# Optimization experiments

Hardware: AMD Instinct MI355X
Metric: run time of the kernel (lower is better)

## Reference

```python
import jax, jax.numpy as jnp
import numpy as np


def _lstm_cell(gates, c_prev):
    # PyTorch gate order: input, forget, cell(g), output
    i, f, g, o = jnp.split(gates, 4, axis=-1)
    c = jax.nn.sigmoid(f) * c_prev + jax.nn.sigmoid(i) * jnp.tanh(g)
    h = jax.nn.sigmoid(o) * jnp.tanh(c)
    return h, c


def setup_inputs() -> dict:
    key = jax.random.key(0)
    ks = jax.random.split(key, 20)
    s = 0.1
    x = jax.random.normal(ks[0], (1, 1, 37), dtype=jnp.float32)
    # active flags live at columns 12 + 5*opp_id; set opponents 0,2,3 active (==1)
    act_idx = 12 + 5 * jnp.arange(5)
    flags = jnp.array([1.0, 0.0, 1.0, 1.0, 0.0], dtype=jnp.float32)
    x = x.at[0, 0, act_idx].set(flags)
    inp = {
        'x': x,
        'gen_Wih': s * jax.random.normal(ks[1], (10, 40, 12), dtype=jnp.float32),
        'gen_Whh': s * jax.random.normal(ks[2], (10, 40, 10), dtype=jnp.float32),
        'gen_bih': s * jax.random.normal(ks[3], (10, 40), dtype=jnp.float32),
        'gen_bhh': s * jax.random.normal(ks[4], (10, 40), dtype=jnp.float32),
        'gen_h0': s * jax.random.normal(ks[5], (10, 10), dtype=jnp.float32),
        'gen_c0': s * jax.random.normal(ks[6], (10, 10), dtype=jnp.float32),
        'game_Wih': s * jax.random.normal(ks[7], (5, 10, 20, 4), dtype=jnp.float32),
        'game_Whh': s * jax.random.normal(ks[8], (5, 10, 20, 5), dtype=jnp.float32),
        'game_bih': s * jax.random.normal(ks[9], (5, 10, 20), dtype=jnp.float32),
        'game_bhh': s * jax.random.normal(ks[10], (5, 10, 20), dtype=jnp.float32),
        'game_h0': s * jax.random.normal(ks[11], (5, 10, 5), dtype=jnp.float32),
        'game_c0': s * jax.random.normal(ks[12], (5, 10, 5), dtype=jnp.float32),
        'W1': s * jax.random.normal(ks[13], (50, 200), dtype=jnp.float32),
        'b1': s * jax.random.normal(ks[14], (50,), dtype=jnp.float32),
        'W2': s * jax.random.normal(ks[15], (10, 50), dtype=jnp.float32),
        'b2': s * jax.random.normal(ks[16], (10,), dtype=jnp.float32),
        'W3': s * jax.random.normal(ks[17], (1, 10), dtype=jnp.float32),
        'b3': s * jax.random.normal(ks[18], (1,), dtype=jnp.float32),
    }
    return inp


def reference(x, gen_Wih, gen_Whh, gen_bih, gen_bhh, gen_h0, gen_c0,
              game_Wih, game_Whh, game_bih, game_bhh, game_h0, game_c0,
              W1, b1, W2, b2, W3, b3):
    # seq_len = batch = 1 (forced by the view(1,1,-1) -> Linear(200) shapes)
    xg = x[0, 0, :12]                                     # [12] general features
    # 10 independent LSTM(12,10) cells, batched via einsum over the cell axis k
    gates_g = (jnp.einsum('kgd,d->kg', gen_Wih, xg)
               + jnp.einsum('kgh,kh->kg', gen_Whh, gen_h0)
               + gen_bih + gen_bhh)                       # [10, 40]
    h_gen, _ = _lstm_cell(gates_g, gen_c0)                # [10, 10]
    x_gen_out = h_gen.reshape(-1)                         # [100]

    xo = x[0, 0, 12:37].reshape(5, 5)                     # 5 opponents x 5 feats
    active = xo[:, 0]                                     # active flag
    feats = xo[:, 1:]                                     # [5, 4]
    # 5 opponents x 10 independent LSTM(4,5) game cells
    gates_o = (jnp.einsum('okgd,od->okg', game_Wih, feats)
               + jnp.einsum('okgh,okh->okg', game_Whh, game_h0)
               + game_bih + game_bhh)                     # [5, 10, 20]
    h_game, _ = _lstm_cell(gates_o, game_c0)              # [5, 10, 5]
    game_flat = h_game.reshape(5, 50)
    # Bug replicated from source: the round loop concatenates x_opp_game (the
    # stale output of game-LSTM #9) 10 times; round LSTM outputs are unused.
    repeated = jnp.tile(h_game[:, 9, :], (1, 10))         # [5, 50]
    opp_single = jnp.concatenate([game_flat, repeated], axis=1)  # [5, 100]

    mask = (active == 1.0).astype(x.dtype)                # 'if x_active == 1'
    opp_avg = (mask[:, None] * opp_single).sum(0) / mask.sum()   # mean over active

    test = jnp.concatenate([x_gen_out, opp_avg])          # [200]
    h1 = jnp.tanh(test @ W1.T + b1)
    h2 = jnp.tanh(h1 @ W2.T + b2)
    out = jnp.tanh(h2 @ W3.T + b3)
    return out.reshape(1, 1, 1)
```

## Files before the change

kernel.cpp:

```cpp
#include <hip/hip_runtime.h>
#include <math.h>


__device__ __forceinline__ float fsig(float v) {
    return __fdividef(1.0f, 1.0f + __expf(-v));
}
__device__ __forceinline__ float ftanh(float v) {
    return 1.0f - __fdividef(2.0f, 1.0f + __expf(2.0f * v));
}

__global__ __launch_bounds__(384) void net6max_kernel(
    const float* __restrict__ x,
    const float* __restrict__ gen_Wih,
    const float* __restrict__ gen_Whh,
    const float* __restrict__ gen_bih,
    const float* __restrict__ gen_bhh,
    const float* __restrict__ gen_h0,
    const float* __restrict__ gen_c0,
    const float* __restrict__ game_Wih,
    const float* __restrict__ game_Whh,
    const float* __restrict__ game_bih,
    const float* __restrict__ game_bhh,
    const float* __restrict__ game_h0,
    const float* __restrict__ game_c0,
    const float* __restrict__ W1,
    const float* __restrict__ b1,
    const float* __restrict__ W2,
    const float* __restrict__ b2,
    const float* __restrict__ W3,
    const float* __restrict__ b3,
    float* __restrict__ out)
{
    __shared__ __align__(16) float s_hgame[5][10][5];
    __shared__ __align__(16) float s_test[200];
    __shared__ __align__(16) float s_h1[52];

    const int tid = threadIdx.x;

    if (tid < 100) {
        int k = tid / 10, j = tid % 10;
        const float*  Wk  = gen_Wih + (size_t)k * 480;
        const float*  Uk  = gen_Whh + (size_t)k * 400;
        const float*  bi  = gen_bih + k * 40;
        const float*  bh  = gen_bhh + k * 40;
        const float2* h02 = (const float2*)(gen_h0 + k * 10);
        float2 h0a = h02[0], h0b = h02[1], h0c = h02[2], h0d = h02[3], h0e = h02[4];
        float4 xa = *(const float4*)&x[0];
        float4 xb = *(const float4*)&x[4];
        float4 xc = *(const float4*)&x[8];
        float g4[4];
        #pragma unroll
        for (int gq = 0; gq < 4; ++gq) {
            int r = gq * 10 + j;
            const float4* w4 = (const float4*)(Wk + r * 12);
            const float2* u2 = (const float2*)(Uk + r * 10);
            float4 p = w4[0] * xa + w4[1] * xb + w4[2] * xc;
            float2 q = u2[0] * h0a + u2[1] * h0b + u2[2] * h0c
                     + u2[3] * h0d + u2[4] * h0e;
            g4[gq] = bi[r] + bh[r] + p.x + p.y + p.z + p.w + q.x + q.y;
        }
        float c = fsig(g4[1]) * gen_c0[tid] + fsig(g4[0]) * ftanh(g4[2]);
        s_test[tid] = fsig(g4[3]) * ftanh(c);
    } else if (tid >= 128 && tid < 378) {
        int u = tid - 128;
        int o = u / 50;
        int rem = u % 50;
        int k = rem / 5, j = rem % 5;
        int ok = o * 10 + k;
        const float* Wk = game_Wih + (size_t)ok * 80;
        const float* Uk = game_Whh + (size_t)ok * 100;
        const float* bi = game_bih + ok * 20;
        const float* bh = game_bhh + ok * 20;
        const float* h0 = game_h0 + ok * 5;
        float h00 = h0[0], h01 = h0[1], h02_ = h0[2], h03 = h0[3], h04 = h0[4];
        const float* fx = x + 13 + 5 * o;
        float f0 = fx[0], f1 = fx[1], f2 = fx[2], f3 = fx[3];
        float g4[4];
        #pragma unroll
        for (int gq = 0; gq < 4; ++gq) {
            int r = gq * 5 + j;
            float4 w = *(const float4*)(Wk + r * 4);
            const float* uu = Uk + r * 5;
            float acc = bi[r] + bh[r]
                      + w.x * f0 + w.y * f1 + w.z * f2 + w.w * f3;
            acc += uu[0]*h00 + uu[1]*h01 + uu[2]*h02_ + uu[3]*h03 + uu[4]*h04;
            g4[gq] = acc;
        }
        float c = fsig(g4[1]) * game_c0[ok * 5 + j] + fsig(g4[0]) * ftanh(g4[2]);
        s_hgame[o][k][j] = fsig(g4[3]) * ftanh(c);
    }
    __syncthreads();

    if (tid < 100) {
        float msum = 0.0f, acc = 0.0f;
        #pragma unroll
        for (int o = 0; o < 5; ++o) {
            float m = (x[12 + 5 * o] == 1.0f) ? 1.0f : 0.0f;
            msum += m;
            float v = (tid < 50) ? s_hgame[o][tid / 5][tid % 5]
                                 : s_hgame[o][9][tid % 5];
            acc += m * v;
        }
        s_test[100 + tid] = __fdividef(acc, msum);
    }
    __syncthreads();

    if (tid < 200) {
        int r = tid >> 2, q = tid & 3;
        const float4* w4 = (const float4*)(W1 + (size_t)r * 200);
        const float4* t4 = (const float4*)s_test;
        float4 acc4 = make_float4(0.f, 0.f, 0.f, 0.f);
        #pragma unroll
        for (int m = 0; m < 12; ++m) {
            int c4 = q + 4 * m;
            acc4 += w4[c4] * t4[c4];
        }
        if (q < 2) {
            int c4 = 48 + q;
            acc4 += w4[c4] * t4[c4];
        }
        float acc = acc4.x + acc4.y + acc4.z + acc4.w;
        acc += __shfl_xor(acc, 1);
        acc += __shfl_xor(acc, 2);
        if (q == 0) s_h1[r] = ftanh(acc + b1[r]);
    }
    __syncthreads();

    if (tid < 32) {
        float acc = 0.f;
        if (tid < 20) {
            int r = tid >> 1, q = tid & 1;
            const float2* w2 = (const float2*)(W2 + (size_t)r * 50);
            const float2* h1v = (const float2*)s_h1;
            float2 acc2 = make_float2(0.f, 0.f);
            #pragma unroll
            for (int m = 0; m < 12; ++m) {
                int c = q + 2 * m;
                acc2 += w2[c] * h1v[c];
            }
            if (q == 0) acc2 += w2[24] * h1v[24];
            float a = acc2.x + acc2.y;
            a += __shfl_xor(a, 1);
            acc = (q == 0) ? ftanh(a + b2[r]) * W3[r] : 0.f;
        }
        acc += __shfl_xor(acc, 2);
        acc += __shfl_xor(acc, 4);
        acc += __shfl_xor(acc, 8);
        acc += __shfl_xor(acc, 16);
        acc += __shfl_xor(acc, 1);
        if (tid == 0) out[0] = ftanh(acc + b3[0]);
    }
}

extern "C" void kernel_launch(void* const* d_in, const int* in_sizes, int n_in,
                              void* d_out, int out_size, void* d_ws, size_t ws_size,
                              hipStream_t stream) {
    (void)in_sizes; (void)n_in; (void)out_size; (void)d_ws; (void)ws_size;
    const float* x        = (const float*)d_in[0];
    const float* gen_Wih  = (const float*)d_in[1];
    const float* gen_Whh  = (const float*)d_in[2];
    const float* gen_bih  = (const float*)d_in[3];
    const float* gen_bhh  = (const float*)d_in[4];
    const float* gen_h0   = (const float*)d_in[5];
    const float* gen_c0   = (const float*)d_in[6];
    const float* game_Wih = (const float*)d_in[7];
    const float* game_Whh = (const float*)d_in[8];
    const float* game_bih = (const float*)d_in[9];
    const float* game_bhh = (const float*)d_in[10];
    const float* game_h0  = (const float*)d_in[11];
    const float* game_c0  = (const float*)d_in[12];
    const float* W1       = (const float*)d_in[13];
    const float* b1       = (const float*)d_in[14];
    const float* W2       = (const float*)d_in[15];
    const float* b2       = (const float*)d_in[16];
    const float* W3       = (const float*)d_in[17];
    const float* b3       = (const float*)d_in[18];
    float* out = (float*)d_out;

    net6max_kernel<<<1, 384, 0, stream>>>(
        x, gen_Wih, gen_Whh, gen_bih, gen_bhh, gen_h0, gen_c0,
        game_Wih, game_Whh, game_bih, game_bhh, game_h0, game_c0,
        W1, b1, W2, b2, W3, b3, out);
}
```

Before: 9.558 us.

## Split LSTM gate computations across more threads with shuffle-based combination

Gen-LSTM cells now use one thread per gate (4 per cell) and game-LSTM cells use two threads per cell, combining the gate results through wavefront shuffles. The block grows from 384 to 960 threads. The goal is a shorter serial dependency chain per thread in the latency-bound first phase, since each thread now loads fewer weight rows. The cost is more wavefronts to schedule and sync, plus extra shuffle instructions.

```diff
diff --git a/kernel.cpp b/kernel.cpp
--- a/kernel.cpp
+++ b/kernel.cpp
@@ -9,7 +9,7 @@
     return 1.0f - __fdividef(2.0f, 1.0f + __expf(2.0f * v));
 }
 
-__global__ __launch_bounds__(384) void net6max_kernel(
+__global__ __launch_bounds__(960) void net6max_kernel(
     const float* __restrict__ x,
     const float* __restrict__ gen_Wih,
     const float* __restrict__ gen_Whh,
@@ -37,36 +37,44 @@
 
     const int tid = threadIdx.x;
 
-    if (tid < 100) {
-        int k = tid / 10, j = tid % 10;
-        const float*  Wk  = gen_Wih + (size_t)k * 480;
-        const float*  Uk  = gen_Whh + (size_t)k * 400;
-        const float*  bi  = gen_bih + k * 40;
-        const float*  bh  = gen_bhh + k * 40;
+    if (tid < 400) {
+        int cell = tid >> 2, gq = tid & 3;
+        int k = cell / 10, j = cell % 10;
+        int r = gq * 10 + j;
+        int row = k * 40 + r;
+        const float4* w4 = (const float4*)(gen_Wih + (size_t)row * 12);
+        const float2* u2 = (const float2*)(gen_Whh + (size_t)row * 10);
         const float2* h02 = (const float2*)(gen_h0 + k * 10);
-        float2 h0a = h02[0], h0b = h02[1], h0c = h02[2], h0d = h02[3], h0e = h02[4];
         float4 xa = *(const float4*)&x[0];
         float4 xb = *(const float4*)&x[4];
         float4 xc = *(const float4*)&x[8];
-        float g4[4];
-        #pragma unroll
-        for (int gq = 0; gq < 4; ++gq) {
-            int r = gq * 10 + j;
-            const float4* w4 = (const float4*)(Wk + r * 12);
-            const float2* u2 = (const float2*)(Uk + r * 10);
-            float4 p = w4[0] * xa + w4[1] * xb + w4[2] * xc;
-            float2 q = u2[0] * h0a + u2[1] * h0b + u2[2] * h0c
-                     + u2[3] * h0d + u2[4] * h0e;
-            g4[gq] = bi[r] + bh[r] + p.x + p.y + p.z + p.w + q.x + q.y;
+        float4 p = w4[0] * xa + w4[1] * xb + w4[2] * xc;
+        float2 q = u2[0] * h02[0] + u2[1] * h02[1] + u2[2] * h02[2]
+                 + u2[3] * h02[3] + u2[4] * h02[4];
+        float gate = gen_bih[row] + gen_bhh[row]
+                   + p.x + p.y + p.z + p.w + q.x + q.y;
+        bool isg = (gq == 2);
+        float a = isg ? 2.0f * gate : -gate;
+        float D = __fdividef(1.0f, 1.0f + __expf(a));
+        float v = isg ? 1.0f - 2.0f * D : D;
+        float c0v = gen_c0[cell];
+        float w = __shfl_xor(v, 2);
+        float pp = (gq == 1) ? v * c0v : v * w;
+        float r1 = __shfl_xor(pp, 1);
+        float r2 = __shfl_xor(w, 1);
+        if (gq == 0) {
+            float c = pp + r1;
+            s_test[cell] = ftanh(c) * r2;
         }
-        float c = fsig(g4[1]) * gen_c0[tid] + fsig(g4[0]) * ftanh(g4[2]);
-        s_test[tid] = fsig(g4[3]) * ftanh(c);
-    } else if (tid >= 128 && tid < 378) {
-        int u = tid - 128;
-        int o = u / 50;
-        int rem = u % 50;
+    } else if (tid >= 448 && tid < 948) {
+        int u = tid - 448;
+        int idx = u >> 1, q = u & 1;
+        int o = idx / 50;
+        int rem = idx % 50;
         int k = rem / 5, j = rem % 5;
         int ok = o * 10 + k;
+        int rA = q * 5 + j;
+        int rB = rA + 10;
         const float* Wk = game_Wih + (size_t)ok * 80;
         const float* Uk = game_Whh + (size_t)ok * 100;
         const float* bi = game_bih + ok * 20;
@@ -75,19 +83,24 @@
         float h00 = h0[0], h01 = h0[1], h02_ = h0[2], h03 = h0[3], h04 = h0[4];
         const float* fx = x + 13 + 5 * o;
         float f0 = fx[0], f1 = fx[1], f2 = fx[2], f3 = fx[3];
-        float g4[4];
-        #pragma unroll
-        for (int gq = 0; gq < 4; ++gq) {
-            int r = gq * 5 + j;
-            float4 w = *(const float4*)(Wk + r * 4);
-            const float* uu = Uk + r * 5;
-            float acc = bi[r] + bh[r]
-                      + w.x * f0 + w.y * f1 + w.z * f2 + w.w * f3;
-            acc += uu[0]*h00 + uu[1]*h01 + uu[2]*h02_ + uu[3]*h03 + uu[4]*h04;
-            g4[gq] = acc;
+        float4 wA = *(const float4*)(Wk + rA * 4);
+        float4 wB = *(const float4*)(Wk + rB * 4);
+        const float* uA = Uk + rA * 5;
+        const float* uB = Uk + rB * 5;
+        float gA = bi[rA] + bh[rA] + wA.x*f0 + wA.y*f1 + wA.z*f2 + wA.w*f3
+                 + uA[0]*h00 + uA[1]*h01 + uA[2]*h02_ + uA[3]*h03 + uA[4]*h04;
+        float gB = bi[rB] + bh[rB] + wB.x*f0 + wB.y*f1 + wB.z*f2 + wB.w*f3
+                 + uB[0]*h00 + uB[1]*h01 + uB[2]*h02_ + uB[3]*h03 + uB[4]*h04;
+        float vA = fsig(gA);
+        float vB = q ? fsig(gB) : ftanh(gB);
+        float c0v = game_c0[ok * 5 + j];
+        float a = q ? vA * c0v : vA * vB;
+        float s1 = __shfl_xor(a, 1);
+        float s2 = __shfl_xor(vB, 1);
+        if (q == 0) {
+            float c = a + s1;
+            s_hgame[o][k][j] = ftanh(c) * s2;
         }
-        float c = fsig(g4[1]) * game_c0[ok * 5 + j] + fsig(g4[0]) * ftanh(g4[2]);
-        s_hgame[o][k][j] = fsig(g4[3]) * ftanh(c);
     }
     __syncthreads();
 
@@ -177,7 +190,7 @@
     const float* b3       = (const float*)d_in[18];
     float* out = (float*)d_out;
 
-    net6max_kernel<<<1, 384, 0, stream>>>(
+    net6max_kernel<<<1, 960, 0, stream>>>(
         x, gen_Wih, gen_Whh, gen_bih, gen_bhh, gen_h0, gen_c0,
         game_Wih, game_Whh, game_bih, game_bhh, game_h0, game_c0,
         W1, b1, W2, b2, W3, b3, out);
```

Measured after the change: 10.18 us. +6.5%, slower.
